# Performance work log

Measured on AMD Instinct MI355X. Metric: run time of the kernel, lower is better.

The kernel has to match this reference:

```python
import jax, jax.numpy as jnp
import numpy as np

B, C, H, W = 256, 512, 14, 14  # C = rnn_size
S = 7                          # spp_size

def setup_inputs() -> dict:
    key = jax.random.key(0)
    ks = jax.random.split(key, 8)
    sd = 1.0 / np.sqrt(C)
    return {
        "att_v": jax.random.normal(ks[0], (B, C, H, W), dtype=jnp.float32),
        "h": jax.random.normal(ks[1], (B, C), dtype=jnp.float32),
        # a2a: Linear(rnn_size, rnn_size)
        "Wa": jax.random.uniform(ks[2], (C, C), jnp.float32, -sd, sd),
        "ba": jax.random.uniform(ks[3], (C,), jnp.float32, -sd, sd),
        # h2a: Linear(rnn_size, rnn_size)
        "Wh": jax.random.uniform(ks[4], (C, C), jnp.float32, -sd, sd),
        "bh": jax.random.uniform(ks[5], (C,), jnp.float32, -sd, sd),
        # d2d: Linear(rnn_size, 1)
        "Wd": jax.random.uniform(ks[6], (C,), jnp.float32, -sd, sd),
        "bd": jax.random.uniform(ks[7], (1,), jnp.float32, -sd, sd),
    }

def reference(att_v, h, Wa, ba, Wh, bh, Wd, bd):
    b, c, hh, ww = att_v.shape
    # AdaptiveAvgPool2d(S) with H,W divisible by S -> block mean
    pooled = att_v.reshape(b, c, S, hh // S, S, ww // S).mean(axis=(3, 5))  # [B,C,S,S]
    a = pooled.reshape(b, c, S * S).transpose(0, 2, 1)  # [B, N=49, C]
    av = jnp.einsum('bnc,dc->bnd', a, Wa) + ba          # a2a, torch Linear: x @ W.T + b
    ah = h @ Wh.T + bh                                  # h2a, [B,C]
    dot = jnp.tanh(av + ah[:, None, :])                 # broadcast add + tanh
    scores = jnp.einsum('bnd,d->bn', dot, Wd) + bd[0]   # d2d -> [B, N]
    weight = jax.nn.softmax(scores, axis=-1)            # over attention positions
    att_res = jnp.einsum('bnc,bn->bc', a, weight)       # bmm(att^T, weight)
    return att_res
```

## Files before the change

kernel.cpp:

```cpp
#include <hip/hip_runtime.h>
#include <hip/hip_bf16.h>

#define BATCH 256
#define CDIM  512
#define NPOS  49
#define MROWS 12544
#define ASTRIDE 520

typedef __attribute__((ext_vector_type(8))) short bf16x8_t;
typedef __attribute__((ext_vector_type(4))) float f32x4_t;

#define WS_NEED 13960192u

__device__ __forceinline__ void load_lds16(const void* g, void* l) {
    __builtin_amdgcn_global_load_lds(
        (const __attribute__((address_space(1))) void*)g,
        (__attribute__((address_space(3))) void*)l, 16, 0, 0);
}

__global__ __launch_bounds__(256, 6) void k1_pool_prep_ah(
    const float* __restrict__ att_v,
    const float* __restrict__ h,
    const float* __restrict__ Wa,
    const float* __restrict__ Wh,
    const float* __restrict__ ba, const float* __restrict__ bh,
    __hip_bfloat16* __restrict__ pooled,
    __hip_bfloat16* __restrict__ Wab,
    float* __restrict__ ahb,
    float* __restrict__ scores,
    int* __restrict__ counters) {
    __shared__ float4 lds4[32 * 49];
    const int bid = blockIdx.x;
    const int t   = threadIdx.x;

    if (bid < 16) {
        ((float4*)scores)[bid * 256 + t] = (float4){0.f, 0.f, 0.f, 0.f};
    } else if (bid == 16) {
        if (t < 64) ((float4*)counters)[t] = (float4){0.f, 0.f, 0.f, 0.f};
    } else if (bid < 273) {
        const int idx = (bid - 17) * 256 + t;
        float4 v = ((const float4*)Wa)[idx];
        Wab[idx * 4 + 0] = __float2bfloat16(v.x);
        Wab[idx * 4 + 1] = __float2bfloat16(v.y);
        Wab[idx * 4 + 2] = __float2bfloat16(v.z);
        Wab[idx * 4 + 3] = __float2bfloat16(v.w);
    } else if (bid < 305) {
        const int rel = bid - 273;
        const int mt = rel & 3;
        const int nt = rel >> 2;
        const int m0 = mt * 64, n0 = nt * 64;
        __hip_bfloat16* aT = (__hip_bfloat16*)lds4;
        __hip_bfloat16* bT = (__hip_bfloat16*)lds4 + 2048;
        const int wave = t >> 6, lane = t & 63;
        const int wm = wave & 1, wn = wave >> 1;
        const int q = lane >> 4, r = lane & 15;
        const int row = t >> 2, cseg = (t & 3) * 8;
        const float* hg = h  + (size_t)(m0 + row) * CDIM + cseg;
        const float* wg = Wh + (size_t)(n0 + row) * CDIM + cseg;

        f32x4_t acc[2][2];
        #pragma unroll
        for (int rt = 0; rt < 2; ++rt)
            #pragma unroll
            for (int ct = 0; ct < 2; ++ct) acc[rt][ct] = (f32x4_t){0.f, 0.f, 0.f, 0.f};

        for (int ks = 0; ks < 16; ++ks) {
            float4 a0 = *(const float4*)(hg + ks * 32);
            float4 a1 = *(const float4*)(hg + ks * 32 + 4);
            float4 b0 = *(const float4*)(wg + ks * 32);
            float4 b1 = *(const float4*)(wg + ks * 32 + 4);
            union { bf16x8_t v; __hip_bfloat16 e[8]; } ua, ub;
            ua.e[0] = __float2bfloat16(a0.x); ua.e[1] = __float2bfloat16(a0.y);
            ua.e[2] = __float2bfloat16(a0.z); ua.e[3] = __float2bfloat16(a0.w);
            ua.e[4] = __float2bfloat16(a1.x); ua.e[5] = __float2bfloat16(a1.y);
            ua.e[6] = __float2bfloat16(a1.z); ua.e[7] = __float2bfloat16(a1.w);
            ub.e[0] = __float2bfloat16(b0.x); ub.e[1] = __float2bfloat16(b0.y);
            ub.e[2] = __float2bfloat16(b0.z); ub.e[3] = __float2bfloat16(b0.w);
            ub.e[4] = __float2bfloat16(b1.x); ub.e[5] = __float2bfloat16(b1.y);
            ub.e[6] = __float2bfloat16(b1.z); ub.e[7] = __float2bfloat16(b1.w);
            __syncthreads();
            *(bf16x8_t*)&aT[row * 32 + cseg] = ua.v;
            *(bf16x8_t*)&bT[row * 32 + cseg] = ub.v;
            __syncthreads();
            bf16x8_t af[2], bf[2];
            #pragma unroll
            for (int rt = 0; rt < 2; ++rt)
                af[rt] = *(const bf16x8_t*)&aT[(wm * 32 + rt * 16 + r) * 32 + q * 8];
            #pragma unroll
            for (int ct = 0; ct < 2; ++ct)
                bf[ct] = *(const bf16x8_t*)&bT[(wn * 32 + ct * 16 + r) * 32 + q * 8];
            #pragma unroll
            for (int rt = 0; rt < 2; ++rt)
                #pragma unroll
                for (int ct = 0; ct < 2; ++ct)
                    acc[rt][ct] = __builtin_amdgcn_mfma_f32_16x16x32_bf16(
                        af[rt], bf[ct], acc[rt][ct], 0, 0, 0);
        }
        #pragma unroll
        for (int ct = 0; ct < 2; ++ct) {
            const int col = n0 + wn * 32 + ct * 16 + r;
            const float bias = ba[col] + bh[col];
            #pragma unroll
            for (int rt = 0; rt < 2; ++rt)
                #pragma unroll
                for (int rg = 0; rg < 4; ++rg) {
                    const int orow = m0 + wm * 32 + rt * 16 + q * 4 + rg;
                    ahb[(size_t)orow * CDIM + col] = acc[rt][ct][rg] + bias;
                }
        }
    } else {
        const int rel = bid - 305;
        const int b  = rel >> 4;
        const int cg = rel & 15;
        const float4* src = (const float4*)(att_v + ((size_t)b * CDIM + cg * 32) * 196);
        #pragma unroll
        for (int k = 0; k < 7; ++k) {
            int idx = t + k * 256;
            if (idx < 1568) lds4[idx] = src[idx];
        }
        __syncthreads();
        const int i = t >> 5;
        const int c = t & 31;
        if (i < 7) {
            const float4* fp = &lds4[c * 49 + 7 * i];
            float4 f0 = fp[0], f1 = fp[1], f2 = fp[2], f3 = fp[3];
            float4 f4 = fp[4], f5 = fp[5], f6 = fp[6];
            float p[7];
            p[0] = f0.x + f0.y + f3.z + f3.w;
            p[1] = f0.z + f0.w + f4.x + f4.y;
            p[2] = f1.x + f1.y + f4.z + f4.w;
            p[3] = f1.z + f1.w + f5.x + f5.y;
            p[4] = f2.x + f2.y + f5.z + f5.w;
            p[5] = f2.z + f2.w + f6.x + f6.y;
            p[6] = f3.x + f3.y + f6.z + f6.w;
            __hip_bfloat16* outp =
                pooled + ((size_t)b * NPOS + i * 7) * CDIM + cg * 32 + c;
            #pragma unroll
            for (int j = 0; j < 7; ++j)
                outp[(size_t)j * CDIM] = __float2bfloat16(p[j] * 0.25f);
        }
    }
}

__global__ __launch_bounds__(256, 4) void gemm_score_fused2(
    const __hip_bfloat16* __restrict__ A,
    const __hip_bfloat16* __restrict__ Bw,
    const float* __restrict__ ahb,
    const float* __restrict__ Wd,
    float* __restrict__ scores,
    int* __restrict__ counters,
    float* __restrict__ out) {
    __shared__ __hip_bfloat16 aT[2 * 64 * 32];
    __shared__ __hip_bfloat16 bT[2 * 128 * 32];
    __shared__ float s_raw[NPOS];
    __shared__ float w_w[NPOS];
    __shared__ int   last_flag;
    const int b  = blockIdx.x >> 2;
    const int nt = blockIdx.x & 3;
    const int t = threadIdx.x;
    const int wave = t >> 6, lane = t & 63;
    const int wm = wave & 1, wn = wave >> 1;
    const int q = lane >> 4, r = lane & 15;
    const int m0 = b * NPOS;
    const int n0 = nt * 128;

    const int srow = t >> 2;
    const int sseg = (t & 3) ^ ((t >> 3) & 3);
    const __hip_bfloat16* Ag  = A  + (size_t)(m0 + srow) * CDIM + sseg * 8;
    const __hip_bfloat16* Bg0 = Bw + (size_t)(n0 + srow) * CDIM + sseg * 8;
    const __hip_bfloat16* Bg1 = Bw + (size_t)(n0 + 64 + srow) * CDIM + sseg * 8;
    char* aD = (char*)aT + t * 16;
    char* bD = (char*)bT + t * 16;

    f32x4_t acc[2][4];
    #pragma unroll
    for (int rt = 0; rt < 2; ++rt)
        #pragma unroll
        for (int ct = 0; ct < 4; ++ct) acc[rt][ct] = (f32x4_t){0.f, 0.f, 0.f, 0.f};

    for (int ks = 0; ks < 8; ++ks) {
        const int k0 = ks * 64;
        load_lds16(Ag + k0, aD);
        load_lds16(Ag + k0 + 32, aD + 4096);
        load_lds16(Bg0 + k0, bD);
        load_lds16(Bg1 + k0, bD + 4096);
        load_lds16(Bg0 + k0 + 32, bD + 8192);
        load_lds16(Bg1 + k0 + 32, bD + 12288);
        __syncthreads();
        #pragma unroll
        for (int s = 0; s < 2; ++s) {
            const __hip_bfloat16* aS = aT + s * 2048;
            const __hip_bfloat16* bS = bT + s * 4096;
            bf16x8_t af[2], bf[4];
            #pragma unroll
            for (int rt = 0; rt < 2; ++rt) {
                const int ar = wm * 32 + rt * 16 + r;
                af[rt] = *(const bf16x8_t*)&aS[ar * 32 + (q ^ ((ar >> 1) & 3)) * 8];
            }
            #pragma unroll
            for (int ct = 0; ct < 4; ++ct) {
                const int br = wn * 64 + ct * 16 + r;
                bf[ct] = *(const bf16x8_t*)&bS[br * 32 + (q ^ ((br >> 1) & 3)) * 8];
            }
            #pragma unroll
            for (int rt = 0; rt < 2; ++rt)
                #pragma unroll
                for (int ct = 0; ct < 4; ++ct)
                    acc[rt][ct] = __builtin_amdgcn_mfma_f32_16x16x32_bf16(
                        af[rt], bf[ct], acc[rt][ct], 0, 0, 0);
        }
        __syncthreads();
    }

    float rsum[2][4];
    #pragma unroll
    for (int rt = 0; rt < 2; ++rt)
        #pragma unroll
        for (int rg = 0; rg < 4; ++rg) rsum[rt][rg] = 0.f;

    const float* ahp = ahb + (size_t)b * CDIM;
    #pragma unroll
    for (int ct = 0; ct < 4; ++ct) {
        const int col = n0 + wn * 64 + ct * 16 + r;
        const float ah = ahp[col];
        const float wd = Wd[col];
        #pragma unroll
        for (int rt = 0; rt < 2; ++rt)
            #pragma unroll
            for (int rg = 0; rg < 4; ++rg) {
                float x = acc[rt][ct][rg] + ah;
                float e = __expf(2.f * x);
                rsum[rt][rg] += (1.f - 2.f / (e + 1.f)) * wd;
            }
    }
    #pragma unroll
    for (int m = 1; m < 16; m <<= 1)
        #pragma unroll
        for (int rt = 0; rt < 2; ++rt)
            #pragma unroll
            for (int rg = 0; rg < 4; ++rg)
                rsum[rt][rg] += __shfl_xor(rsum[rt][rg], m, 64);
    if (r == 0) {
        float* sb = scores + b * 64;
        #pragma unroll
        for (int rt = 0; rt < 2; ++rt)
            #pragma unroll
            for (int rg = 0; rg < 4; ++rg) {
                const int row = wm * 32 + rt * 16 + q * 4 + rg;
                if (row < NPOS) atomicAdd(&sb[row], rsum[rt][rg]);
            }
    }

    asm volatile("s_waitcnt vmcnt(0)" ::: "memory");
    __syncthreads();
    if (t == 0) last_flag = (atomicAdd(&counters[b], 1) == 3);
    __syncthreads();
    if (!last_flag) return;

    if (t < NPOS) s_raw[t] = atomicAdd(&scores[b * 64 + t], 0.0f);
    __syncthreads();
    if (t < NPOS) {
        float vmax = -3.0e38f;
        #pragma unroll
        for (int n = 0; n < NPOS; ++n) vmax = fmaxf(vmax, s_raw[n]);
        float S = 0.f;
        #pragma unroll
        for (int n = 0; n < NPOS; ++n) S += __expf(s_raw[n] - vmax);
        w_w[t] = __expf(s_raw[t] - vmax) / S;
    }
    __syncthreads();

    const __hip_bfloat16* Ap = A + (size_t)m0 * CDIM;
    float a0 = 0.f, a1 = 0.f;
    #pragma unroll
    for (int n = 0; n < NPOS; ++n) {
        const float w = w_w[n];
        a0 += w * __bfloat162float(Ap[(size_t)n * CDIM + t]);
        a1 += w * __bfloat162float(Ap[(size_t)n * CDIM + t + 256]);
    }
    out[b * CDIM + t]       = a0;
    out[b * CDIM + t + 256] = a1;
}

__global__ void prep_convert(const float* __restrict__ Wa,
                             const float* __restrict__ Wh,
                             __hip_bfloat16* __restrict__ Wab,
                             __hip_bfloat16* __restrict__ Whb) {
    int gid = blockIdx.x * blockDim.x + threadIdx.x;
    const int quarter = (CDIM * CDIM) / 4;
    const float4* src; __hip_bfloat16* dst; int idx;
    if (gid < quarter) { src = (const float4*)Wa; dst = Wab; idx = gid; }
    else               { src = (const float4*)Wh; dst = Whb; idx = gid - quarter; }
    float4 v = src[idx];
    dst[idx * 4 + 0] = __float2bfloat16(v.x);
    dst[idx * 4 + 1] = __float2bfloat16(v.y);
    dst[idx * 4 + 2] = __float2bfloat16(v.z);
    dst[idx * 4 + 3] = __float2bfloat16(v.w);
}

__global__ __launch_bounds__(512, 2) void att_spp_main(
    const float* __restrict__ att_v, const float* __restrict__ h,
    const float* __restrict__ ba, const float* __restrict__ bh,
    const float* __restrict__ Wd,
    const __hip_bfloat16* __restrict__ Wab, const __hip_bfloat16* __restrict__ Whb,
    float* __restrict__ out) {
    __shared__ __hip_bfloat16 a_lds[64 * ASTRIDE];
    __shared__ __hip_bfloat16 h_lds[CDIM];
    __shared__ float babh_lds[CDIM];
    __shared__ float wd_lds[CDIM];
    __shared__ float scores_lds[64];
    __shared__ float weights_lds[NPOS];
    const int b = blockIdx.x, t = threadIdx.x;
    h_lds[t]    = __float2bfloat16(h[b * CDIM + t]);
    babh_lds[t] = ba[t] + bh[t];
    wd_lds[t]   = Wd[t];
    if (t < 64) scores_lds[t] = 0.f;
    for (int idx = t; idx < (64 - NPOS) * ASTRIDE; idx += 512)
        a_lds[NPOS * ASTRIDE + idx] = __float2bfloat16(0.f);
    {
        const int jj = t & 7, g = t >> 3;
        const float2* att2 = (const float2*)(att_v + (size_t)b * CDIM * 196);
        if (jj < 7) {
            for (int ci = 0; ci < 8; ++ci) {
                const int c = g + (ci << 6), cbase = c * 98;
                #pragma unroll
                for (int i = 0; i < 7; ++i) {
                    float2 v0 = att2[cbase + i * 14 + jj];
                    float2 v1 = att2[cbase + i * 14 + 7 + jj];
                    a_lds[(i * 7 + jj) * ASTRIDE + c] =
                        __float2bfloat16((v0.x + v0.y + v1.x + v1.y) * 0.25f);
                }
            }
        }
    }
    __syncthreads();
    const int wave = t >> 6, lane = t & 63, q = lane >> 4, r = lane & 15;
    f32x4_t acc[4][4];
    #pragma unroll
    for (int rt = 0; rt < 4; ++rt)
        #pragma unroll
        for (int ct = 0; ct < 4; ++ct) acc[rt][ct] = (f32x4_t){0.f,0.f,0.f,0.f};
    const int dBase = wave * 64 + r;
    for (int ks = 0; ks < 16; ++ks) {
        const int k0 = ks * 32 + q * 8;
        bf16x8_t af[4], bf[4];
        #pragma unroll
        for (int rt = 0; rt < 4; ++rt)
            af[rt] = *(const bf16x8_t*)&a_lds[(rt * 16 + r) * ASTRIDE + k0];
        #pragma unroll
        for (int ct = 0; ct < 4; ++ct)
            bf[ct] = *(const bf16x8_t*)&Wab[(size_t)(dBase + ct * 16) * CDIM + k0];
        #pragma unroll
        for (int rt = 0; rt < 4; ++rt)
            #pragma unroll
            for (int ct = 0; ct < 4; ++ct)
                acc[rt][ct] = __builtin_amdgcn_mfma_f32_16x16x32_bf16(
                    af[rt], bf[ct], acc[rt][ct], 0, 0, 0);
    }
    for (int ks = 0; ks < 16; ++ks) {
        const int k0 = ks * 32 + q * 8;
        bf16x8_t af = *(const bf16x8_t*)&h_lds[k0];
        bf16x8_t bf[4];
        #pragma unroll
        for (int ct = 0; ct < 4; ++ct)
            bf[ct] = *(const bf16x8_t*)&Whb[(size_t)(dBase + ct * 16) * CDIM + k0];
        #pragma unroll
        for (int rt = 0; rt < 4; ++rt)
            #pragma unroll
            for (int ct = 0; ct < 4; ++ct)
                acc[rt][ct] = __builtin_amdgcn_mfma_f32_16x16x32_bf16(
                    af, bf[ct], acc[rt][ct], 0, 0, 0);
    }
    float part[4][4];
    #pragma unroll
    for (int rt = 0; rt < 4; ++rt)
        #pragma unroll
        for (int rg = 0; rg < 4; ++rg) part[rt][rg] = 0.f;
    #pragma unroll
    for (int ct = 0; ct < 4; ++ct) {
        const int d = dBase + ct * 16;
        const float bias = babh_lds[d], wd = wd_lds[d];
        #pragma unroll
        for (int rt = 0; rt < 4; ++rt)
            #pragma unroll
            for (int rg = 0; rg < 4; ++rg) {
                float x = acc[rt][ct][rg] + bias;
                float e = __expf(2.f * x);
                part[rt][rg] += (1.f - 2.f / (e + 1.f)) * wd;
            }
    }
    #pragma unroll
    for (int m = 1; m < 16; m <<= 1)
        #pragma unroll
        for (int rt = 0; rt < 4; ++rt)
            #pragma unroll
            for (int rg = 0; rg < 4; ++rg)
                part[rt][rg] += __shfl_xor(part[rt][rg], m, 64);
    if (r == 0) {
        #pragma unroll
        for (int rt = 0; rt < 4; ++rt)
            #pragma unroll
            for (int rg = 0; rg < 4; ++rg)
                atomicAdd(&scores_lds[rt * 16 + q * 4 + rg], part[rt][rg]);
    }
    __syncthreads();
    if (wave == 0) {
        float v = (lane < NPOS) ? scores_lds[lane] : -3.0e38f;
        float vmax = v;
        #pragma unroll
        for (int m = 1; m < 64; m <<= 1) vmax = fmaxf(vmax, __shfl_xor(vmax, m, 64));
        float e = (lane < NPOS) ? __expf(v - vmax) : 0.f;
        float s = e;
        #pragma unroll
        for (int m = 1; m < 64; m <<= 1) s += __shfl_xor(s, m, 64);
        if (lane < NPOS) weights_lds[lane] = e / s;
    }
    __syncthreads();
    float sum = 0.f;
    #pragma unroll
    for (int n = 0; n < NPOS; ++n)
        sum += __bfloat162float(a_lds[n * ASTRIDE + t]) * weights_lds[n];
    out[b * CDIM + t] = sum;
}

extern "C" void kernel_launch(void* const* d_in, const int* in_sizes, int n_in,
                              void* d_out, int out_size, void* d_ws, size_t ws_size,
                              hipStream_t stream) {
    const float* att_v = (const float*)d_in[0];
    const float* h     = (const float*)d_in[1];
    const float* Wa    = (const float*)d_in[2];
    const float* ba    = (const float*)d_in[3];
    const float* Wh    = (const float*)d_in[4];
    const float* bh    = (const float*)d_in[5];
    const float* Wd    = (const float*)d_in[6];

    if (ws_size >= WS_NEED) {
        char* ws = (char*)d_ws;
        __hip_bfloat16* Wab     = (__hip_bfloat16*)(ws);
        __hip_bfloat16* pooled  = (__hip_bfloat16*)(ws + 524288);
        float*          ahb     = (float*)(ws + 13369344);
        float*          scores  = (float*)(ws + 13893632);
        int*            counters= (int*)(ws + 13959168);

        k1_pool_prep_ah<<<4401, 256, 0, stream>>>(att_v, h, Wa, Wh, ba, bh,
                                                  pooled, Wab, ahb,
                                                  scores, counters);
        gemm_score_fused2<<<1024, 256, 0, stream>>>(pooled, Wab, ahb, Wd,
                                                    scores, counters,
                                                    (float*)d_out);
    } else {
        __hip_bfloat16* Wab = (__hip_bfloat16*)d_ws;
        __hip_bfloat16* Whb = Wab + (size_t)CDIM * CDIM;
        prep_convert<<<512, 256, 0, stream>>>(Wa, Wh, Wab, Whb);
        att_spp_main<<<BATCH, 512, 0, stream>>>(att_v, h, ba, bh, Wd, Wab, Whb,
                                                (float*)d_out);
    }
}
```

Baseline: 187.4 us.

## Pre-swizzle pooled and Wa into MFMA fragment layout, drop LDS staging in GEMM

The prep kernel now writes both the pooled activations and the bf16 Wa into a fragment-major layout that matches the 16x16x32 MFMA operand order, padding each batch to 64 rows. The GEMM kernel then loads operand fragments straight from global memory with one coalesced 16-byte load per lane, with no LDS staging and no __syncthreads. The pooling path also uses direct global-to-LDS loads and an LDS transpose so its stores are vectorised. The cost is a larger workspace, since the padded rows add memory traffic, and more reliance on L2 to serve operand reuse across waves.

```diff
diff --git a/kernel.cpp b/kernel.cpp
--- a/kernel.cpp
+++ b/kernel.cpp
@@ -4,13 +4,12 @@
 #define BATCH 256
 #define CDIM  512
 #define NPOS  49
-#define MROWS 12544
 #define ASTRIDE 520
 
 typedef __attribute__((ext_vector_type(8))) short bf16x8_t;
 typedef __attribute__((ext_vector_type(4))) float f32x4_t;
 
-#define WS_NEED 13960192u
+#define WS_NEED 17892352u
 
 __device__ __forceinline__ void load_lds16(const void* g, void* l) {
     __builtin_amdgcn_global_load_lds(
@@ -29,7 +28,7 @@
     float* __restrict__ ahb,
     float* __restrict__ scores,
     int* __restrict__ counters) {
-    __shared__ float4 lds4[32 * 49];
+    __shared__ char smem[25088];
     const int bid = blockIdx.x;
     const int t   = threadIdx.x;
 
@@ -37,20 +36,35 @@
         ((float4*)scores)[bid * 256 + t] = (float4){0.f, 0.f, 0.f, 0.f};
     } else if (bid == 16) {
         if (t < 64) ((float4*)counters)[t] = (float4){0.f, 0.f, 0.f, 0.f};
-    } else if (bid < 273) {
-        const int idx = (bid - 17) * 256 + t;
-        float4 v = ((const float4*)Wa)[idx];
-        Wab[idx * 4 + 0] = __float2bfloat16(v.x);
-        Wab[idx * 4 + 1] = __float2bfloat16(v.y);
-        Wab[idx * 4 + 2] = __float2bfloat16(v.z);
-        Wab[idx * 4 + 3] = __float2bfloat16(v.w);
-    } else if (bid < 305) {
-        const int rel = bid - 273;
+    } else if (bid < 49) {
+        const int cg2 = bid - 17;
+        __hip_bfloat16* wl = (__hip_bfloat16*)smem;
+        const float4* wsrc = (const float4*)(Wa + (size_t)cg2 * 16 * CDIM);
+        #pragma unroll
+        for (int k = 0; k < 8; ++k) {
+            const int idx = t + k * 256;
+            float4 v = wsrc[idx];
+            const int d = idx >> 7, cf = (idx & 127) * 4;
+            __hip_bfloat16* w = &wl[d * 520 + cf];
+            w[0] = __float2bfloat16(v.x); w[1] = __float2bfloat16(v.y);
+            w[2] = __float2bfloat16(v.z); w[3] = __float2bfloat16(v.w);
+        }
+        __syncthreads();
+        #pragma unroll
+        for (int e = 0; e < 4; ++e) {
+            const int chunk = t + e * 256;
+            const int kb = chunk >> 6, lane = chunk & 63;
+            bf16x8_t v = *(const bf16x8_t*)
+                &wl[(lane & 15) * 520 + kb * 32 + (lane >> 4) * 8];
+            *(bf16x8_t*)&Wab[(size_t)cg2 * 8192 + chunk * 8] = v;
+        }
+    } else if (bid < 81) {
+        const int rel = bid - 49;
         const int mt = rel & 3;
         const int nt = rel >> 2;
         const int m0 = mt * 64, n0 = nt * 64;
-        __hip_bfloat16* aT = (__hip_bfloat16*)lds4;
-        __hip_bfloat16* bT = (__hip_bfloat16*)lds4 + 2048;
+        __hip_bfloat16* aT = (__hip_bfloat16*)smem;
+        __hip_bfloat16* bT = (__hip_bfloat16*)smem + 2048;
         const int wave = t >> 6, lane = t & 63;
         const int wm = wave & 1, wn = wave >> 1;
         const int q = lane >> 4, r = lane & 15;
@@ -109,23 +123,23 @@
                 }
         }
     } else {
-        const int rel = bid - 305;
+        const int rel = bid - 81;
         const int b  = rel >> 4;
         const int cg = rel & 15;
         const float4* src = (const float4*)(att_v + ((size_t)b * CDIM + cg * 32) * 196);
         #pragma unroll
         for (int k = 0; k < 7; ++k) {
-            int idx = t + k * 256;
-            if (idx < 1568) lds4[idx] = src[idx];
+            const int idx = t + k * 256;
+            if (idx < 1568) load_lds16(src + idx, smem + idx * 16);
         }
         __syncthreads();
         const int i = t >> 5;
         const int c = t & 31;
+        float p[7];
         if (i < 7) {
-            const float4* fp = &lds4[c * 49 + 7 * i];
+            const float4* fp = (const float4*)smem + (c * 49 + 7 * i);
             float4 f0 = fp[0], f1 = fp[1], f2 = fp[2], f3 = fp[3];
             float4 f4 = fp[4], f5 = fp[5], f6 = fp[6];
-            float p[7];
             p[0] = f0.x + f0.y + f3.z + f3.w;
             p[1] = f0.z + f0.w + f4.x + f4.y;
             p[2] = f1.x + f1.y + f4.z + f4.w;
@@ -133,16 +147,30 @@
             p[4] = f2.x + f2.y + f5.z + f5.w;
             p[5] = f2.z + f2.w + f6.x + f6.y;
             p[6] = f3.x + f3.y + f6.z + f6.w;
+        }
+        __syncthreads();
+        __hip_bfloat16* pl = (__hip_bfloat16*)smem;
+        if (i < 7) {
+            #pragma unroll
+            for (int j = 0; j < 7; ++j)
+                pl[c * 65 + i * 7 + j] = __float2bfloat16(p[j] * 0.25f);
+        }
+        __syncthreads();
+        {
+            const int rg = t >> 6, lane = t & 63;
+            const int m = lane & 15, qd = lane >> 4;
+            union { bf16x8_t v; __hip_bfloat16 e[8]; } u;
+            #pragma unroll
+            for (int e = 0; e < 8; ++e)
+                u.e[e] = pl[(qd * 8 + e) * 65 + rg * 16 + m];
             __hip_bfloat16* outp =
-                pooled + ((size_t)b * NPOS + i * 7) * CDIM + cg * 32 + c;
-            #pragma unroll
-            for (int j = 0; j < 7; ++j)
-                outp[(size_t)j * CDIM] = __float2bfloat16(p[j] * 0.25f);
-        }
-    }
-}
-
-__global__ __launch_bounds__(256, 4) void gemm_score_fused2(
+                pooled + ((((size_t)b * 16 + cg) * 4 + rg) << 9) + lane * 8;
+            *(bf16x8_t*)outp = u.v;
+        }
+    }
+}
+
+__global__ __launch_bounds__(256, 4) void gemm_score_direct(
     const __hip_bfloat16* __restrict__ A,
     const __hip_bfloat16* __restrict__ Bw,
     const float* __restrict__ ahb,
@@ -150,8 +178,6 @@
     float* __restrict__ scores,
     int* __restrict__ counters,
     float* __restrict__ out) {
-    __shared__ __hip_bfloat16 aT[2 * 64 * 32];
-    __shared__ __hip_bfloat16 bT[2 * 128 * 32];
     __shared__ float s_raw[NPOS];
     __shared__ float w_w[NPOS];
     __shared__ int   last_flag;
@@ -161,16 +187,10 @@
     const int wave = t >> 6, lane = t & 63;
     const int wm = wave & 1, wn = wave >> 1;
     const int q = lane >> 4, r = lane & 15;
-    const int m0 = b * NPOS;
     const int n0 = nt * 128;
 
-    const int srow = t >> 2;
-    const int sseg = (t & 3) ^ ((t >> 3) & 3);
-    const __hip_bfloat16* Ag  = A  + (size_t)(m0 + srow) * CDIM + sseg * 8;
-    const __hip_bfloat16* Bg0 = Bw + (size_t)(n0 + srow) * CDIM + sseg * 8;
-    const __hip_bfloat16* Bg1 = Bw + (size_t)(n0 + 64 + srow) * CDIM + sseg * 8;
-    char* aD = (char*)aT + t * 16;
-    char* bD = (char*)bT + t * 16;
+    const __hip_bfloat16* Ab = A + ((size_t)b << 15);
+    const __hip_bfloat16* Bb = Bw + ((size_t)(nt * 8 + wn * 4) << 13);
 
     f32x4_t acc[2][4];
     #pragma unroll
@@ -178,38 +198,21 @@
         #pragma unroll
         for (int ct = 0; ct < 4; ++ct) acc[rt][ct] = (f32x4_t){0.f, 0.f, 0.f, 0.f};
 
-    for (int ks = 0; ks < 8; ++ks) {
-        const int k0 = ks * 64;
-        load_lds16(Ag + k0, aD);
-        load_lds16(Ag + k0 + 32, aD + 4096);
-        load_lds16(Bg0 + k0, bD);
-        load_lds16(Bg1 + k0, bD + 4096);
-        load_lds16(Bg0 + k0 + 32, bD + 8192);
-        load_lds16(Bg1 + k0 + 32, bD + 12288);
-        __syncthreads();
-        #pragma unroll
-        for (int s = 0; s < 2; ++s) {
-            const __hip_bfloat16* aS = aT + s * 2048;
-            const __hip_bfloat16* bS = bT + s * 4096;
-            bf16x8_t af[2], bf[4];
-            #pragma unroll
-            for (int rt = 0; rt < 2; ++rt) {
-                const int ar = wm * 32 + rt * 16 + r;
-                af[rt] = *(const bf16x8_t*)&aS[ar * 32 + (q ^ ((ar >> 1) & 3)) * 8];
-            }
-            #pragma unroll
-            for (int ct = 0; ct < 4; ++ct) {
-                const int br = wn * 64 + ct * 16 + r;
-                bf[ct] = *(const bf16x8_t*)&bS[br * 32 + (q ^ ((br >> 1) & 3)) * 8];
-            }
-            #pragma unroll
-            for (int rt = 0; rt < 2; ++rt)
-                #pragma unroll
-                for (int ct = 0; ct < 4; ++ct)
-                    acc[rt][ct] = __builtin_amdgcn_mfma_f32_16x16x32_bf16(
-                        af[rt], bf[ct], acc[rt][ct], 0, 0, 0);
-        }
-        __syncthreads();
+    #pragma unroll 4
+    for (int kb = 0; kb < 16; ++kb) {
+        bf16x8_t af[2], bf[4];
+        #pragma unroll
+        for (int rt = 0; rt < 2; ++rt)
+            af[rt] = *(const bf16x8_t*)&Ab[((kb * 4 + wm * 2 + rt) << 9) + lane * 8];
+        #pragma unroll
+        for (int ct = 0; ct < 4; ++ct)
+            bf[ct] = *(const bf16x8_t*)&Bb[(((ct << 4) + kb) << 9) + lane * 8];
+        #pragma unroll
+        for (int rt = 0; rt < 2; ++rt)
+            #pragma unroll
+            for (int ct = 0; ct < 4; ++ct)
+                acc[rt][ct] = __builtin_amdgcn_mfma_f32_16x16x32_bf16(
+                    af[rt], bf[ct], acc[rt][ct], 0, 0, 0);
     }
 
     float rsum[2][4];
@@ -270,16 +273,21 @@
     }
     __syncthreads();
 
-    const __hip_bfloat16* Ap = A + (size_t)m0 * CDIM;
-    float a0 = 0.f, a1 = 0.f;
-    #pragma unroll
-    for (int n = 0; n < NPOS; ++n) {
-        const float w = w_w[n];
-        a0 += w * __bfloat162float(Ap[(size_t)n * CDIM + t]);
-        a1 += w * __bfloat162float(Ap[(size_t)n * CDIM + t + 256]);
-    }
-    out[b * CDIM + t]       = a0;
-    out[b * CDIM + t + 256] = a1;
+    {
+        const int c0 = t, c1 = t + 256;
+        const int k0 = ((c0 >> 5) << 11) + (((c0 >> 3) & 3) << 7) + (c0 & 7);
+        const int k1 = ((c1 >> 5) << 11) + (((c1 >> 3) & 3) << 7) + (c1 & 7);
+        float a0 = 0.f, a1 = 0.f;
+        #pragma unroll
+        for (int n = 0; n < NPOS; ++n) {
+            const float w = w_w[n];
+            const int ro = ((n >> 4) << 9) + ((n & 15) << 3);
+            a0 += w * __bfloat162float(Ab[k0 + ro]);
+            a1 += w * __bfloat162float(Ab[k1 + ro]);
+        }
+        out[b * CDIM + c0] = a0;
+        out[b * CDIM + c1] = a1;
+    }
 }
 
 __global__ void prep_convert(const float* __restrict__ Wa,
@@ -438,14 +446,14 @@
         char* ws = (char*)d_ws;
         __hip_bfloat16* Wab     = (__hip_bfloat16*)(ws);
         __hip_bfloat16* pooled  = (__hip_bfloat16*)(ws + 524288);
-        float*          ahb     = (float*)(ws + 13369344);
-        float*          scores  = (float*)(ws + 13893632);
-        int*            counters= (int*)(ws + 13959168);
-
-        k1_pool_prep_ah<<<4401, 256, 0, stream>>>(att_v, h, Wa, Wh, ba, bh,
+        float*          ahb     = (float*)(ws + 17301504);
+        float*          scores  = (float*)(ws + 17825792);
+        int*            counters= (int*)(ws + 17891328);
+
+        k1_pool_prep_ah<<<4177, 256, 0, stream>>>(att_v, h, Wa, Wh, ba, bh,
                                                   pooled, Wab, ahb,
                                                   scores, counters);
-        gemm_score_fused2<<<1024, 256, 0, stream>>>(pooled, Wab, ahb, Wd,
+        gemm_score_direct<<<1024, 256, 0, stream>>>(pooled, Wab, ahb, Wd,
                                                     scores, counters,
                                                     (float*)d_out);
     } else {
```

Measured after the change: 193.0 us. 1.03x slower.
